# Kernel optimization log

Measured on AMD Instinct MI355X. Metric: run time of the kernel, lower is better.

Reference implementation:

```python
import jax, jax.numpy as jnp
import numpy as np

N_NODES = 50000
N_EDGES = 800000
IN_DIM = 128
OUT_DIM = 64


def setup_inputs() -> dict:
    key = jax.random.key(0)
    k1, k2, k3, k4 = jax.random.split(key, 4)
    x = jax.random.normal(k1, (N_NODES, IN_DIM), dtype=jnp.float32)
    edge_index = jax.random.randint(k2, (2, N_EDGES), 0, N_NODES, dtype=jnp.int64)
    # learned params: W: Linear(in_dim, out_dim, bias=False); att: Linear(2*out_dim, 1, bias=False)
    W = jax.random.normal(k3, (IN_DIM, OUT_DIM), dtype=jnp.float32) * 0.05
    att = jax.random.normal(k4, (2 * OUT_DIM, 1), dtype=jnp.float32) * 0.05
    return {"x": x, "edge_index": edge_index, "W": W, "att": att}


def reference(x, edge_index, W, att):
    n = x.shape[0]
    h = x @ W  # [N, D]
    src, dst = edge_index[0], edge_index[1]
    # per-edge attention logit: leaky_relu(att^T [h_src ; h_dst])
    e = jnp.concatenate([h[src], h[dst]], axis=-1) @ att  # [E, 1]
    e = jax.nn.leaky_relu(e[:, 0], negative_slope=0.2)  # [E]
    # segment softmax over edges grouped by destination node
    m = jax.ops.segment_max(e, dst, num_segments=n)  # [N]
    ex = jnp.exp(e - m[dst])  # [E]
    denom = jax.ops.segment_sum(ex, dst, num_segments=n)  # [N]
    alpha = ex / denom[dst]  # [E]
    # weighted scatter-add aggregation
    agg = jax.ops.segment_sum(alpha[:, None] * h[src], dst, num_segments=n)  # [N, D]
    return jax.nn.elu(agg)
```

## Files before the change

kernel.cpp:

```cpp
#include <hip/hip_runtime.h>
#include <hip/hip_bf16.h>
#include <hip/hip_fp16.h>
#include <math.h>

#define N_NODES 50000
#define N_EDGES 800000
#define IN_DIM 128
#define OUT_DIM 64

typedef __attribute__((ext_vector_type(8))) short bf16x8;
typedef __attribute__((ext_vector_type(4))) float f32x4;

static __device__ __forceinline__ ushort f2bf(float f) {
  uint u = __float_as_uint(f);
  uint r = (u + 0x7fffu + ((u >> 16) & 1u)) >> 16;
  return (ushort)r;
}
static __device__ __forceinline__ float bf2f(ushort h) {
  return __uint_as_float(((uint)h) << 16);
}

#define N4 (N_NODES / 4)
#define SCAN_NB ((N4 + 255) / 256)
#define GEMM_NB ((N_NODES + 63) / 64)
#define K2_T (N_EDGES / 8)
#define K4_T (N_EDGES / 8)

__global__ __launch_bounds__(256) void k0_prep(const float* __restrict__ W,
                                               int* __restrict__ deg,
                                               ushort* __restrict__ WTfrag) {
  int t = blockIdx.x * 256 + threadIdx.x;
  if (t < N4) ((int4*)deg)[t] = make_int4(0, 0, 0, 0);
  if (t < IN_DIM * OUT_DIM) {
    int j = t & 7, l = (t >> 3) & 63, ks = (t >> 9) & 3, nt = (t >> 11) & 3;
    int c = nt * 16 + (l & 15);
    int k = ks * 32 + ((l >> 4) << 3) + j;
    WTfrag[t] = f2bf(W[(size_t)k * OUT_DIM + c]);
  }
}

__global__ __launch_bounds__(256) void k1_mfma(
    const float* __restrict__ x, const ushort* __restrict__ WTfrag,
    const float* __restrict__ att,
    __half* __restrict__ h, float* __restrict__ a1, float* __restrict__ a2) {
  __shared__ __align__(16) ushort Ah[64 * 128];
  __shared__ __align__(16) ushort Al[64 * 128];

  int tid = threadIdx.x;
  int row0 = blockIdx.x * 64;

#pragma unroll
  for (int it = 0; it < 8; ++it) {
    int i4 = it * 256 + tid;
    int row = i4 >> 5;
    int kq = i4 & 31;
    int grow = row0 + row;
    if (grow > N_NODES - 1) grow = N_NODES - 1;
    float4 v = ((const float4*)x)[(size_t)grow * 32 + kq];
    ushort4 hi, lo;
    hi.x = f2bf(v.x); lo.x = f2bf(v.x - bf2f(hi.x));
    hi.y = f2bf(v.y); lo.y = f2bf(v.y - bf2f(hi.y));
    hi.z = f2bf(v.z); lo.z = f2bf(v.z - bf2f(hi.z));
    hi.w = f2bf(v.w); lo.w = f2bf(v.w - bf2f(hi.w));
    int idx = (row * 128 + kq * 4) ^ ((row & 7) << 3);
    *(ushort4*)&Ah[idx] = hi;
    *(ushort4*)&Al[idx] = lo;
  }
  __syncthreads();

  int w = tid >> 6, l = tid & 63;
  int ml = l & 15, kg = l >> 4;
  const bf16x8* __restrict__ Bf = (const bf16x8*)WTfrag;

  f32x4 acc[4];
#pragma unroll
  for (int nt = 0; nt < 4; ++nt) acc[nt] = (f32x4){0.f, 0.f, 0.f, 0.f};

#pragma unroll
  for (int ks = 0; ks < 4; ++ks) {
    int arow = w * 16 + ml;
    int aidx = (arow * 128 + ks * 32 + kg * 8) ^ ((arow & 7) << 3);
    bf16x8 a_h = *(const bf16x8*)&Ah[aidx];
    bf16x8 a_l = *(const bf16x8*)&Al[aidx];
#pragma unroll
    for (int nt = 0; nt < 4; ++nt) {
      bf16x8 b = Bf[(nt * 4 + ks) * 64 + l];
      acc[nt] = __builtin_amdgcn_mfma_f32_16x16x32_bf16(a_h, b, acc[nt], 0, 0, 0);
      acc[nt] = __builtin_amdgcn_mfma_f32_16x16x32_bf16(a_l, b, acc[nt], 0, 0, 0);
    }
  }

  float t1[4], t2[4];
#pragma unroll
  for (int nt = 0; nt < 4; ++nt) {
    t1[nt] = att[nt * 16 + ml];
    t2[nt] = att[OUT_DIM + nt * 16 + ml];
  }
#pragma unroll
  for (int r = 0; r < 4; ++r) {
    int drow = kg * 4 + r;
    int grow = row0 + w * 16 + drow;
    bool ok = grow < N_NODES;
    float p1 = 0.f, p2 = 0.f;
#pragma unroll
    for (int nt = 0; nt < 4; ++nt) {
      float d = acc[nt][r];
      if (ok) h[(size_t)grow * OUT_DIM + nt * 16 + ml] = __float2half(d);
      p1 = fmaf(d, t1[nt], p1);
      p2 = fmaf(d, t2[nt], p2);
    }
#pragma unroll
    for (int o = 1; o <= 8; o <<= 1) {
      p1 += __shfl_xor(p1, o, 64);
      p2 += __shfl_xor(p2, o, 64);
    }
    if (ml == 0 && ok) { a1[grow] = p1; a2[grow] = p2; }
  }
}

__global__ __launch_bounds__(256) void k2_rank(const int* __restrict__ dstp,
                                               int* __restrict__ deg,
                                               int* __restrict__ rank) {
  int t = blockIdx.x * 256 + threadIdx.x;
  if (t >= K2_T) return;
  int4 d0 = ((const int4*)dstp)[t * 2];
  int4 d1 = ((const int4*)dstp)[t * 2 + 1];
  int4 r0, r1;
  r0.x = atomicAdd(&deg[d0.x], 1);
  r0.y = atomicAdd(&deg[d0.y], 1);
  r0.z = atomicAdd(&deg[d0.z], 1);
  r0.w = atomicAdd(&deg[d0.w], 1);
  r1.x = atomicAdd(&deg[d1.x], 1);
  r1.y = atomicAdd(&deg[d1.y], 1);
  r1.z = atomicAdd(&deg[d1.z], 1);
  r1.w = atomicAdd(&deg[d1.w], 1);
  ((int4*)rank)[t * 2] = r0;
  ((int4*)rank)[t * 2 + 1] = r1;
}

__global__ __launch_bounds__(256) void k3a_scan(const int* __restrict__ deg,
                                                int* __restrict__ off,
                                                int* __restrict__ bsum) {
  __shared__ int sw[4];
  int tid = threadIdx.x, lane = tid & 63, wid = tid >> 6;
  int i4 = blockIdx.x * 256 + tid;
  int4 v = make_int4(0, 0, 0, 0);
  if (i4 < N4) v = ((const int4*)deg)[i4];
  int local = v.x + v.y + v.z + v.w;
  int incl = local;
#pragma unroll
  for (int o = 1; o < 64; o <<= 1) {
    int t = __shfl_up(incl, o, 64);
    if (lane >= o) incl += t;
  }
  if (lane == 63) sw[wid] = incl;
  __syncthreads();
  if (tid == 0) {
    int c = 0;
#pragma unroll
    for (int ww = 0; ww < 4; ++ww) { int t = sw[ww]; sw[ww] = c; c += t; }
    bsum[blockIdx.x] = c;
  }
  __syncthreads();
  int excl = incl - local + sw[wid];
  int4 o;
  o.x = excl; o.y = o.x + v.x; o.z = o.y + v.y; o.w = o.z + v.z;
  if (i4 < N4) ((int4*)off)[i4] = o;
}

__global__ __launch_bounds__(256) void k3c_add(int* __restrict__ off,
                                               const int* __restrict__ bsum,
                                               const float* __restrict__ a2,
                                               int2* __restrict__ oa2) {
  __shared__ int sb[64];
  int tid = threadIdx.x;
  if (tid < 64) {
    int v = (tid < SCAN_NB) ? bsum[tid] : 0;
    int incl = v;
#pragma unroll
    for (int o = 1; o < 64; o <<= 1) {
      int t = __shfl_up(incl, o, 64);
      if (tid >= o) incl += t;
    }
    sb[tid] = incl - v;
  }
  __syncthreads();
  int i4 = blockIdx.x * 256 + tid;
  if (i4 == 0) off[N_NODES] = N_EDGES;
  if (i4 >= N4) return;
  int add = sb[blockIdx.x];
  int4 v = ((const int4*)off)[i4];
  v.x += add; v.y += add; v.z += add; v.w += add;
  ((int4*)off)[i4] = v;
  float4 a = ((const float4*)a2)[i4];
  int4 p0 = make_int4(v.x, __float_as_int(a.x), v.y, __float_as_int(a.y));
  int4 p1 = make_int4(v.z, __float_as_int(a.z), v.w, __float_as_int(a.w));
  ((int4*)oa2)[i4 * 2] = p0;
  ((int4*)oa2)[i4 * 2 + 1] = p1;
}

__global__ __launch_bounds__(256) void k4_scatter(
    const int* __restrict__ src, const int* __restrict__ dstp,
    const int* __restrict__ rank,
    const float* __restrict__ a1, const int2* __restrict__ oa2,
    int2* __restrict__ sedge) {
  int t = blockIdx.x * 256 + threadIdx.x;
  if (t >= K4_T) return;
  int4 s0 = ((const int4*)src)[t * 2],  s1 = ((const int4*)src)[t * 2 + 1];
  int4 d0 = ((const int4*)dstp)[t * 2], d1 = ((const int4*)dstp)[t * 2 + 1];
  int4 r0 = ((const int4*)rank)[t * 2], r1 = ((const int4*)rank)[t * 2 + 1];
  float A[8];
  A[0] = a1[s0.x]; A[1] = a1[s0.y]; A[2] = a1[s0.z]; A[3] = a1[s0.w];
  A[4] = a1[s1.x]; A[5] = a1[s1.y]; A[6] = a1[s1.z]; A[7] = a1[s1.w];
  int2 O[8];
  O[0] = oa2[d0.x]; O[1] = oa2[d0.y]; O[2] = oa2[d0.z]; O[3] = oa2[d0.w];
  O[4] = oa2[d1.x]; O[5] = oa2[d1.y]; O[6] = oa2[d1.z]; O[7] = oa2[d1.w];
  int S[8] = {s0.x, s0.y, s0.z, s0.w, s1.x, s1.y, s1.z, s1.w};
  int R[8] = {r0.x, r0.y, r0.z, r0.w, r1.x, r1.y, r1.z, r1.w};
#pragma unroll
  for (int q = 0; q < 8; ++q) {
    float e = A[q] + __int_as_float(O[q].y);
    e = e > 0.f ? e : 0.2f * e;
    sedge[O[q].x + R[q]] = make_int2(S[q], __float_as_int(__expf(e)));
  }
}

__global__ __launch_bounds__(256) void k5_agg(
    const int* __restrict__ off, const int2* __restrict__ sedge,
    const __half* __restrict__ h, float* __restrict__ out) {
  int tid = threadIdx.x;
  int g = tid >> 3, gl = tid & 7;
  int n = blockIdx.x * 32 + g;
  if (n >= N_NODES) return;
  int b = off[n], e = off[n + 1];

  float sum = 0.f;
  float a0 = 0.f, a1_ = 0.f, a2_ = 0.f, a3 = 0.f;
  float a4 = 0.f, a5 = 0.f, a6 = 0.f, a7 = 0.f;
  const __half* __restrict__ hb = h;

#define K5_ACC(rr, ww)                                                        \
  {                                                                           \
    float2 f;                                                                 \
    f = __half22float2(__builtin_bit_cast(__half2, rr.x));                    \
    a0 = fmaf(ww, f.x, a0); a1_ = fmaf(ww, f.y, a1_);                         \
    f = __half22float2(__builtin_bit_cast(__half2, rr.y));                    \
    a2_ = fmaf(ww, f.x, a2_); a3 = fmaf(ww, f.y, a3);                         \
    f = __half22float2(__builtin_bit_cast(__half2, rr.z));                    \
    a4 = fmaf(ww, f.x, a4); a5 = fmaf(ww, f.y, a5);                           \
    f = __half22float2(__builtin_bit_cast(__half2, rr.w));                    \
    a6 = fmaf(ww, f.x, a6); a7 = fmaf(ww, f.y, a7);                           \
  }

  int j = b;
  for (; j + 7 < e; j += 8) {
    int2 s0 = sedge[j + 0], s1 = sedge[j + 1], s2 = sedge[j + 2], s3 = sedge[j + 3];
    int2 s4 = sedge[j + 4], s5 = sedge[j + 5], s6 = sedge[j + 6], s7 = sedge[j + 7];
    uint4 r0 = ((const uint4*)(hb + (size_t)s0.x * OUT_DIM))[gl];
    uint4 r1 = ((const uint4*)(hb + (size_t)s1.x * OUT_DIM))[gl];
    uint4 r2 = ((const uint4*)(hb + (size_t)s2.x * OUT_DIM))[gl];
    uint4 r3 = ((const uint4*)(hb + (size_t)s3.x * OUT_DIM))[gl];
    uint4 r4 = ((const uint4*)(hb + (size_t)s4.x * OUT_DIM))[gl];
    uint4 r5 = ((const uint4*)(hb + (size_t)s5.x * OUT_DIM))[gl];
    uint4 r6 = ((const uint4*)(hb + (size_t)s6.x * OUT_DIM))[gl];
    uint4 r7 = ((const uint4*)(hb + (size_t)s7.x * OUT_DIM))[gl];
    float w0 = __int_as_float(s0.y), w1 = __int_as_float(s1.y);
    float w2 = __int_as_float(s2.y), w3 = __int_as_float(s3.y);
    float w4 = __int_as_float(s4.y), w5 = __int_as_float(s5.y);
    float w6 = __int_as_float(s6.y), w7 = __int_as_float(s7.y);
    sum += ((w0 + w1) + (w2 + w3)) + ((w4 + w5) + (w6 + w7));
    K5_ACC(r0, w0); K5_ACC(r1, w1); K5_ACC(r2, w2); K5_ACC(r3, w3);
    K5_ACC(r4, w4); K5_ACC(r5, w5); K5_ACC(r6, w6); K5_ACC(r7, w7);
  }
  for (; j + 3 < e; j += 4) {
    int2 s0 = sedge[j + 0], s1 = sedge[j + 1], s2 = sedge[j + 2], s3 = sedge[j + 3];
    uint4 r0 = ((const uint4*)(hb + (size_t)s0.x * OUT_DIM))[gl];
    uint4 r1 = ((const uint4*)(hb + (size_t)s1.x * OUT_DIM))[gl];
    uint4 r2 = ((const uint4*)(hb + (size_t)s2.x * OUT_DIM))[gl];
    uint4 r3 = ((const uint4*)(hb + (size_t)s3.x * OUT_DIM))[gl];
    float w0 = __int_as_float(s0.y), w1 = __int_as_float(s1.y);
    float w2 = __int_as_float(s2.y), w3 = __int_as_float(s3.y);
    sum += (w0 + w1) + (w2 + w3);
    K5_ACC(r0, w0); K5_ACC(r1, w1); K5_ACC(r2, w2); K5_ACC(r3, w3);
  }
  for (; j < e; ++j) {
    int2 s0 = sedge[j];
    uint4 r0 = ((const uint4*)(hb + (size_t)s0.x * OUT_DIM))[gl];
    float w0 = __int_as_float(s0.y);
    sum += w0;
    K5_ACC(r0, w0);
  }

  float inv = (e > b) ? 1.f / sum : 0.f;
  a0 *= inv; a1_ *= inv; a2_ *= inv; a3 *= inv;
  a4 *= inv; a5 *= inv; a6 *= inv; a7 *= inv;
  float4 o0, o1;
  o0.x = a0 > 0.f ? a0 : (__expf(a0) - 1.f);
  o0.y = a1_ > 0.f ? a1_ : (__expf(a1_) - 1.f);
  o0.z = a2_ > 0.f ? a2_ : (__expf(a2_) - 1.f);
  o0.w = a3 > 0.f ? a3 : (__expf(a3) - 1.f);
  o1.x = a4 > 0.f ? a4 : (__expf(a4) - 1.f);
  o1.y = a5 > 0.f ? a5 : (__expf(a5) - 1.f);
  o1.z = a6 > 0.f ? a6 : (__expf(a6) - 1.f);
  o1.w = a7 > 0.f ? a7 : (__expf(a7) - 1.f);
  float4* ob = (float4*)(out + (size_t)n * OUT_DIM);
  ob[gl * 2] = o0;
  ob[gl * 2 + 1] = o1;
}

extern "C" void kernel_launch(void* const* d_in, const int* in_sizes, int n_in,
                              void* d_out, int out_size, void* d_ws, size_t ws_size,
                              hipStream_t stream) {
  const float* x   = (const float*)d_in[0];
  const int*   ei  = (const int*)d_in[1];
  const float* W   = (const float*)d_in[2];
  const float* att = (const float*)d_in[3];
  float* out = (float*)d_out;

  char* p = (char*)d_ws;
  __half* h  = (__half*)p;  p += (size_t)N_NODES * OUT_DIM * sizeof(__half);
  float* a1  = (float*)p;   p += (size_t)N_NODES * sizeof(float);
  float* a2  = (float*)p;   p += (size_t)N_NODES * sizeof(float);
  int*   deg = (int*)p;     p += (size_t)N_NODES * sizeof(int);
  int*   off = (int*)p;     p += (size_t)(N_NODES + 4) * sizeof(int);
  int2*  oa2 = (int2*)p;    p += (size_t)N_NODES * sizeof(int2);
  int*   rank = (int*)p;    p += (size_t)N_EDGES * sizeof(int);
  int2*  sedge = (int2*)p;  p += (size_t)N_EDGES * sizeof(int2);
  int*   bsum = (int*)p;    p += 64 * sizeof(int);
  ushort* WTfrag = (ushort*)p; p += (size_t)OUT_DIM * IN_DIM * sizeof(ushort);

  const int* src  = ei;
  const int* dstp = ei + N_EDGES;

  k0_prep<<<SCAN_NB, 256, 0, stream>>>(W, deg, WTfrag);
  k2_rank<<<(K2_T + 255) / 256, 256, 0, stream>>>(dstp, deg, rank);
  k1_mfma<<<GEMM_NB, 256, 0, stream>>>(x, WTfrag, att, h, a1, a2);
  k3a_scan<<<SCAN_NB, 256, 0, stream>>>(deg, off, bsum);
  k3c_add<<<SCAN_NB, 256, 0, stream>>>(off, bsum, a2, oa2);
  k4_scatter<<<(K4_T + 255) / 256, 256, 0, stream>>>(src, dstp, rank, a1, oa2, sedge);
  k5_agg<<<(N_NODES + 31) / 32, 256, 0, stream>>>(off, sedge, h, out);
}
```

Baseline: 98.39 us.

## Drop split-bf16 GEMM correction and fold scan block-offset add into consumers

The GEMM now converts x to a single bf16 instead of a hi/lo pair, which halves its LDS footprint and MFMA count. It also adds an occupancy hint to the launch bounds. The separate block-offset add kernel and the packed oa2 array are removed. The scatter and aggregation kernels now each rescan the 64 block sums into LDS and add them on the fly. This saves one launch and one round trip over the node arrays, at the cost of lower GEMM precision in h and the attention logits, plus an extra gather of a2 in the scatter.

```diff
diff --git a/kernel.cpp b/kernel.cpp
--- a/kernel.cpp
+++ b/kernel.cpp
@@ -11,13 +11,9 @@
 typedef __attribute__((ext_vector_type(8))) short bf16x8;
 typedef __attribute__((ext_vector_type(4))) float f32x4;
 
-static __device__ __forceinline__ ushort f2bf(float f) {
+static __device__ __forceinline__ uint f2bf(float f) {
   uint u = __float_as_uint(f);
-  uint r = (u + 0x7fffu + ((u >> 16) & 1u)) >> 16;
-  return (ushort)r;
-}
-static __device__ __forceinline__ float bf2f(ushort h) {
-  return __uint_as_float(((uint)h) << 16);
+  return (u + 0x7fffu + ((u >> 16) & 1u)) >> 16;
 }
 
 #define N4 (N_NODES / 4)
@@ -35,16 +31,15 @@
     int j = t & 7, l = (t >> 3) & 63, ks = (t >> 9) & 3, nt = (t >> 11) & 3;
     int c = nt * 16 + (l & 15);
     int k = ks * 32 + ((l >> 4) << 3) + j;
-    WTfrag[t] = f2bf(W[(size_t)k * OUT_DIM + c]);
-  }
-}
-
-__global__ __launch_bounds__(256) void k1_mfma(
+    WTfrag[t] = (ushort)f2bf(W[(size_t)k * OUT_DIM + c]);
+  }
+}
+
+__global__ __launch_bounds__(256, 8) void k1_mfma(
     const float* __restrict__ x, const ushort* __restrict__ WTfrag,
     const float* __restrict__ att,
     __half* __restrict__ h, float* __restrict__ a1, float* __restrict__ a2) {
   __shared__ __align__(16) ushort Ah[64 * 128];
-  __shared__ __align__(16) ushort Al[64 * 128];
 
   int tid = threadIdx.x;
   int row0 = blockIdx.x * 64;
@@ -57,14 +52,10 @@
     int grow = row0 + row;
     if (grow > N_NODES - 1) grow = N_NODES - 1;
     float4 v = ((const float4*)x)[(size_t)grow * 32 + kq];
-    ushort4 hi, lo;
-    hi.x = f2bf(v.x); lo.x = f2bf(v.x - bf2f(hi.x));
-    hi.y = f2bf(v.y); lo.y = f2bf(v.y - bf2f(hi.y));
-    hi.z = f2bf(v.z); lo.z = f2bf(v.z - bf2f(hi.z));
-    hi.w = f2bf(v.w); lo.w = f2bf(v.w - bf2f(hi.w));
+    uint2 hv = make_uint2(f2bf(v.x) | (f2bf(v.y) << 16),
+                          f2bf(v.z) | (f2bf(v.w) << 16));
     int idx = (row * 128 + kq * 4) ^ ((row & 7) << 3);
-    *(ushort4*)&Ah[idx] = hi;
-    *(ushort4*)&Al[idx] = lo;
+    *(uint2*)&Ah[idx] = hv;
   }
   __syncthreads();
 
@@ -81,12 +72,10 @@
     int arow = w * 16 + ml;
     int aidx = (arow * 128 + ks * 32 + kg * 8) ^ ((arow & 7) << 3);
     bf16x8 a_h = *(const bf16x8*)&Ah[aidx];
-    bf16x8 a_l = *(const bf16x8*)&Al[aidx];
 #pragma unroll
     for (int nt = 0; nt < 4; ++nt) {
       bf16x8 b = Bf[(nt * 4 + ks) * 64 + l];
       acc[nt] = __builtin_amdgcn_mfma_f32_16x16x32_bf16(a_h, b, acc[nt], 0, 0, 0);
-      acc[nt] = __builtin_amdgcn_mfma_f32_16x16x32_bf16(a_l, b, acc[nt], 0, 0, 0);
     }
   }
 
@@ -138,9 +127,9 @@
   ((int4*)rank)[t * 2 + 1] = r1;
 }
 
-__global__ __launch_bounds__(256) void k3a_scan(const int* __restrict__ deg,
-                                                int* __restrict__ off,
-                                                int* __restrict__ bsum) {
+__global__ __launch_bounds__(256) void k3_scan(const int* __restrict__ deg,
+                                               int* __restrict__ off,
+                                               int* __restrict__ bsum) {
   __shared__ int sw[4];
   int tid = threadIdx.x, lane = tid & 63, wid = tid >> 6;
   int i4 = blockIdx.x * 256 + tid;
@@ -168,12 +157,8 @@
   if (i4 < N4) ((int4*)off)[i4] = o;
 }
 
-__global__ __launch_bounds__(256) void k3c_add(int* __restrict__ off,
-                                               const int* __restrict__ bsum,
-                                               const float* __restrict__ a2,
-                                               int2* __restrict__ oa2) {
-  __shared__ int sb[64];
-  int tid = threadIdx.x;
+__device__ __forceinline__ void scan_bsum_to_lds(const int* __restrict__ bsum,
+                                                 int* sBX, int tid) {
   if (tid < 64) {
     int v = (tid < SCAN_NB) ? bsum[tid] : 0;
     int incl = v;
@@ -182,57 +167,58 @@
       int t = __shfl_up(incl, o, 64);
       if (tid >= o) incl += t;
     }
-    sb[tid] = incl - v;
+    sBX[tid] = incl - v;
   }
   __syncthreads();
-  int i4 = blockIdx.x * 256 + tid;
-  if (i4 == 0) off[N_NODES] = N_EDGES;
-  if (i4 >= N4) return;
-  int add = sb[blockIdx.x];
-  int4 v = ((const int4*)off)[i4];
-  v.x += add; v.y += add; v.z += add; v.w += add;
-  ((int4*)off)[i4] = v;
-  float4 a = ((const float4*)a2)[i4];
-  int4 p0 = make_int4(v.x, __float_as_int(a.x), v.y, __float_as_int(a.y));
-  int4 p1 = make_int4(v.z, __float_as_int(a.z), v.w, __float_as_int(a.w));
-  ((int4*)oa2)[i4 * 2] = p0;
-  ((int4*)oa2)[i4 * 2 + 1] = p1;
 }
 
 __global__ __launch_bounds__(256) void k4_scatter(
     const int* __restrict__ src, const int* __restrict__ dstp,
-    const int* __restrict__ rank,
-    const float* __restrict__ a1, const int2* __restrict__ oa2,
-    int2* __restrict__ sedge) {
-  int t = blockIdx.x * 256 + threadIdx.x;
+    const int* __restrict__ rank, const int* __restrict__ bsum,
+    const float* __restrict__ a1, const float* __restrict__ a2,
+    const int* __restrict__ off, int2* __restrict__ sedge) {
+  __shared__ int sBX[64];
+  int tid = threadIdx.x;
+  scan_bsum_to_lds(bsum, sBX, tid);
+
+  int t = blockIdx.x * 256 + tid;
   if (t >= K4_T) return;
   int4 s0 = ((const int4*)src)[t * 2],  s1 = ((const int4*)src)[t * 2 + 1];
   int4 d0 = ((const int4*)dstp)[t * 2], d1 = ((const int4*)dstp)[t * 2 + 1];
   int4 r0 = ((const int4*)rank)[t * 2], r1 = ((const int4*)rank)[t * 2 + 1];
-  float A[8];
-  A[0] = a1[s0.x]; A[1] = a1[s0.y]; A[2] = a1[s0.z]; A[3] = a1[s0.w];
-  A[4] = a1[s1.x]; A[5] = a1[s1.y]; A[6] = a1[s1.z]; A[7] = a1[s1.w];
-  int2 O[8];
-  O[0] = oa2[d0.x]; O[1] = oa2[d0.y]; O[2] = oa2[d0.z]; O[3] = oa2[d0.w];
-  O[4] = oa2[d1.x]; O[5] = oa2[d1.y]; O[6] = oa2[d1.z]; O[7] = oa2[d1.w];
   int S[8] = {s0.x, s0.y, s0.z, s0.w, s1.x, s1.y, s1.z, s1.w};
+  int D[8] = {d0.x, d0.y, d0.z, d0.w, d1.x, d1.y, d1.z, d1.w};
   int R[8] = {r0.x, r0.y, r0.z, r0.w, r1.x, r1.y, r1.z, r1.w};
+  float A[8], B[8];
+  int O[8];
 #pragma unroll
   for (int q = 0; q < 8; ++q) {
-    float e = A[q] + __int_as_float(O[q].y);
+    A[q] = a1[S[q]];
+    B[q] = a2[D[q]];
+    O[q] = off[D[q]];
+  }
+#pragma unroll
+  for (int q = 0; q < 8; ++q) {
+    float e = A[q] + B[q];
     e = e > 0.f ? e : 0.2f * e;
-    sedge[O[q].x + R[q]] = make_int2(S[q], __float_as_int(__expf(e)));
+    int p = O[q] + sBX[D[q] >> 10] + R[q];
+    sedge[p] = make_int2(S[q], __float_as_int(__expf(e)));
   }
 }
 
 __global__ __launch_bounds__(256) void k5_agg(
-    const int* __restrict__ off, const int2* __restrict__ sedge,
+    const int* __restrict__ off, const int* __restrict__ bsum,
+    const int2* __restrict__ sedge,
     const __half* __restrict__ h, float* __restrict__ out) {
+  __shared__ int sBX[64];
   int tid = threadIdx.x;
+  scan_bsum_to_lds(bsum, sBX, tid);
+
   int g = tid >> 3, gl = tid & 7;
   int n = blockIdx.x * 32 + g;
   if (n >= N_NODES) return;
-  int b = off[n], e = off[n + 1];
+  int b = off[n] + sBX[n >> 10];
+  int e = (n + 1 < N_NODES) ? (off[n + 1] + sBX[(n + 1) >> 10]) : N_EDGES;
 
   float sum = 0.f;
   float a0 = 0.f, a1_ = 0.f, a2_ = 0.f, a3 = 0.f;
@@ -323,7 +309,6 @@
   float* a2  = (float*)p;   p += (size_t)N_NODES * sizeof(float);
   int*   deg = (int*)p;     p += (size_t)N_NODES * sizeof(int);
   int*   off = (int*)p;     p += (size_t)(N_NODES + 4) * sizeof(int);
-  int2*  oa2 = (int2*)p;    p += (size_t)N_NODES * sizeof(int2);
   int*   rank = (int*)p;    p += (size_t)N_EDGES * sizeof(int);
   int2*  sedge = (int2*)p;  p += (size_t)N_EDGES * sizeof(int2);
   int*   bsum = (int*)p;    p += 64 * sizeof(int);
@@ -335,8 +320,7 @@
   k0_prep<<<SCAN_NB, 256, 0, stream>>>(W, deg, WTfrag);
   k2_rank<<<(K2_T + 255) / 256, 256, 0, stream>>>(dstp, deg, rank);
   k1_mfma<<<GEMM_NB, 256, 0, stream>>>(x, WTfrag, att, h, a1, a2);
-  k3a_scan<<<SCAN_NB, 256, 0, stream>>>(deg, off, bsum);
-  k3c_add<<<SCAN_NB, 256, 0, stream>>>(off, bsum, a2, oa2);
-  k4_scatter<<<(K4_T + 255) / 256, 256, 0, stream>>>(src, dstp, rank, a1, oa2, sedge);
-  k5_agg<<<(N_NODES + 31) / 32, 256, 0, stream>>>(off, sedge, h, out);
-}
+  k3_scan<<<SCAN_NB, 256, 0, stream>>>(deg, off, bsum);
+  k4_scatter<<<(K4_T + 255) / 256, 256, 0, stream>>>(src, dstp, rank, bsum, a1, a2, off, sedge);
+  k5_agg<<<(N_NODES + 31) / 32, 256, 0, stream>>>(off, bsum, sedge, h, out);
+}
```

Measured after the change: 99.00 us. No clear change (+0.6%).
